# Kernel optimization log

Measured on AMD Instinct MI355X. Metric: run time of the kernel, lower is better.

The kernel has to match this reference:

```python
import jax, jax.numpy as jnp
import numpy as np

B, C, H, W = 8, 256, 128, 128
NUM_HEADS = 8
EPS = 1e-6


def setup_inputs() -> dict:
    key = jax.random.key(0)
    ks = jax.random.split(key, 7)
    s = 1.0 / np.sqrt(C)
    return {
        "x": jax.random.normal(ks[0], (B, C, H, W), dtype=jnp.float32),
        "Wq": jax.random.normal(ks[1], (C, C), dtype=jnp.float32) * s,
        "bq": jax.random.normal(ks[2], (C,), dtype=jnp.float32) * 0.01,
        "Wk": jax.random.normal(ks[3], (C, C), dtype=jnp.float32) * s,
        "bk": jax.random.normal(ks[4], (C,), dtype=jnp.float32) * 0.01,
        "Wv": jax.random.normal(ks[5], (C, C), dtype=jnp.float32) * s,
        "bv": jax.random.normal(ks[6], (C,), dtype=jnp.float32) * 0.01,
    }


def reference(x, Wq, bq, Wk, bk, Wv, bv):
    b, c_full, h_sp, w_sp = x.shape
    p = NUM_HEADS
    c = c_full // p  # per-head channels
    n = h_sp * w_sp  # spatial tokens

    def proj(Wm, bm):
        # 1x1 conv == channel-mixing linear: out[b,o,h,w] = sum_c W[o,c]*x[b,c,h,w] + b[o]
        return jnp.einsum('bchw,oc->bohw', x, Wm) + bm[None, :, None, None]

    q = jax.nn.softplus(proj(Wq, bq)).reshape(b, p, c, n).transpose(0, 1, 3, 2)  # [b,p,n,c]
    k = jax.nn.softplus(proj(Wk, bk)).reshape(b, p, c, n)                        # [b,p,c,n]
    v = proj(Wv, bv).reshape(b, p, c, n)                                         # [b,p,c,n]

    # KV accumulation: [b,p,c_k,c_v] (small)
    kv = jnp.einsum('bpmn,bpcn->bpmc', k, v)
    # normalization: 1 / (q . (sum_n k + eps))
    norm = 1.0 / jnp.einsum('bpnc,bpc->bpn', q, jnp.sum(k, axis=-1) + EPS)
    out = jnp.einsum('bpnm,bpmc,bpn->bpcn', q, kv, norm)  # [b,p,c,n]
    return out.reshape(b, c_full, h_sp, w_sp)
```

## Files before the change

kernel.cpp:

```cpp
#include <hip/hip_runtime.h>
#include <hip/hip_bf16.h>
#include <math.h>

#define BATCH 8
#define CFULL 256
#define HEADS 8
#define CH 32
#define NTOK 16384
#define TN 64
#define TTN 32
#define KSLD 40
#define EPS 1e-6f

#define SWZ(tok) ((((tok) & 7) << 3) ^ ((((tok) >> 3) & 3) << 6))

typedef __bf16 bf16x8 __attribute__((ext_vector_type(8)));
typedef float f32x4 __attribute__((ext_vector_type(4)));
typedef float f32x16 __attribute__((ext_vector_type(16)));
typedef float fvec4 __attribute__((ext_vector_type(4)));
typedef unsigned short ushort8v __attribute__((ext_vector_type(8)));
typedef int int4v __attribute__((ext_vector_type(4)));

__device__ __forceinline__ unsigned short bf16bits(float f) {
    return __builtin_bit_cast(unsigned short, (__bf16)f);
}
__device__ __forceinline__ float softplus_f(float x) {
    return fmaxf(x, 0.0f) + __logf(1.0f + __expf(-fabsf(x)));
}

__device__ __forceinline__ void quad_transpose(fvec4& a, int lane) {
    const bool o1 = lane & 1, o2 = lane & 2;
    float s1 = o1 ? a.x : a.y; float g1 = __shfl_xor(s1, 1);
    float s2 = o1 ? a.z : a.w; float g2 = __shfl_xor(s2, 1);
    a.x = o1 ? g1 : a.x;  a.y = o1 ? a.y : g1;
    a.z = o1 ? g2 : a.z;  a.w = o1 ? a.w : g2;
    float s3 = o2 ? a.x : a.z; float g3 = __shfl_xor(s3, 2);
    float s4 = o2 ? a.y : a.w; float g4 = __shfl_xor(s4, 2);
    a.x = o2 ? g3 : a.x;  a.z = o2 ? a.z : g3;
    a.y = o2 ? g4 : a.y;  a.w = o2 ? a.w : g4;
}

template <int NW>
__device__ __forceinline__ void stage_x(const float* __restrict__ xb, int n0,
                                        unsigned short* xs, int wv, int lane) {
    const int q4 = lane & 3;
    const int t0 = (lane >> 2) << 2;
    constexpr int G = 64 / NW;
    #pragma unroll
    for (int g = 0; g < G; ++g) {
        const int c0 = wv * (G * 4) + g * 4;
        fvec4 a = __builtin_nontemporal_load(
            (const fvec4*)(xb + (size_t)(c0 + q4) * NTOK + n0 + t0));
        quad_transpose(a, lane);
        ushort4 pk;
        pk.x = bf16bits(a.x); pk.y = bf16bits(a.y);
        pk.z = bf16bits(a.z); pk.w = bf16bits(a.w);
        *(ushort4*)&xs[lane * CFULL + (c0 ^ SWZ(lane))] = pk;
    }
}

template <int NW>
__device__ __forceinline__ void stage_tile(const unsigned short* __restrict__ xTb,
                                           int n0, unsigned short* xs, int wv, int lane) {
    constexpr int R = 64 / NW;
    const unsigned short* src = xTb + (size_t)(n0 + wv * R) * CFULL + lane * 8;
    unsigned short* dst = &xs[wv * R * CFULL];
    #pragma unroll
    for (int i = 0; i < R / 2; ++i) {
        __builtin_amdgcn_global_load_lds(
            (const __attribute__((address_space(1))) unsigned int*)(src + i * 512),
            (__attribute__((address_space(3))) unsigned int*)(dst + i * 512),
            16, 0, 0);
    }
}

__device__ __forceinline__ void stage32(const unsigned short* __restrict__ xTb,
                                        int n0, unsigned short* buf, int wv, int lane) {
    const unsigned short* src = xTb + (size_t)(n0 + wv * 4) * CFULL + lane * 8;
    unsigned short* dst = buf + wv * 4 * CFULL;
    #pragma unroll
    for (int i = 0; i < 2; ++i) {
        __builtin_amdgcn_global_load_lds(
            (const __attribute__((address_space(1))) unsigned int*)(src + i * 512),
            (__attribute__((address_space(3))) unsigned int*)(dst + i * 512),
            16, 0, 0);
    }
}

__global__ void prep_w(const float* __restrict__ Wq, const float* __restrict__ Wk,
                       const float* __restrict__ Wv, unsigned short* __restrict__ dst)
{
    const int i = blockIdx.x * 256 + threadIdx.x;
    const float* src = (i < 65536) ? Wq : ((i < 131072) ? Wk : Wv);
    dst[i] = bf16bits(src[i & 65535]);
}

__global__ __launch_bounds__(512)
void xpose(const float* __restrict__ x, unsigned short* __restrict__ xT)
{
    __shared__ __align__(16) unsigned short xs[TN * CFULL];
    const int tid = threadIdx.x;
    const int lane = tid & 63;
    const int wv = tid >> 6;
    const int b = blockIdx.x >> 8;
    const int n0 = (blockIdx.x & 255) * TN;

    stage_x<8>(x + (size_t)b * CFULL * NTOK, n0, xs, wv, lane);
    __syncthreads();
    int4v* dst = (int4v*)(xT + ((size_t)b * NTOK + n0) * CFULL);
    const int4v* src = (const int4v*)xs;
    #pragma unroll
    for (int i = 0; i < 4; ++i)
        dst[i * 512 + tid] = src[i * 512 + tid];
}

__global__ __launch_bounds__(512)
void k1_kv(const unsigned short* __restrict__ xT,
           const unsigned short* __restrict__ Wk,
           const unsigned short* __restrict__ Wv,
           const float* __restrict__ bk, const float* __restrict__ bv,
           float* __restrict__ kvpart, float* __restrict__ kspart,
           int bpb, int ntiles)
{
    __shared__ __align__(16) unsigned short xs0[TTN * CFULL];
    __shared__ __align__(16) unsigned short xs1[TTN * CFULL];
    __shared__ __align__(16) unsigned short ks[CFULL * KSLD];
    __shared__ __align__(16) unsigned short vs[CFULL * KSLD];

    const int tid = threadIdx.x;
    const int lane = tid & 63;
    const int wv = tid >> 6;
    const int l15 = lane & 15;
    const int lhi = lane >> 4;
    const int bid = blockIdx.x;
    const int b = bid / bpb;
    const int blk = bid % bpb;
    const int tokbase = blk * (ntiles * TTN);
    const unsigned short* xTb = xT + (size_t)b * NTOK * CFULL;

    float bkr[2], bvr[2];
    #pragma unroll
    for (int of = 0; of < 2; ++of) {
        bkr[of] = bk[wv * 32 + of * 16 + l15];
        bvr[of] = bv[wv * 32 + of * 16 + l15];
    }

    f32x16 kvacc = {};
    float ksum[2] = {0.f, 0.f};

    stage32(xTb, tokbase, xs0, wv, lane);
    __syncthreads();

    for (int t = 0; t < ntiles; ++t) {
        unsigned short* cur = (t & 1) ? xs1 : xs0;
        unsigned short* nxt = (t & 1) ? xs0 : xs1;
        if (t + 1 < ntiles)
            stage32(xTb, tokbase + (t + 1) * TTN, nxt, wv, lane);

        {
            f32x4 acc[2][2] = {};
            #pragma unroll
            for (int kk = 0; kk < 8; ++kk) {
                const int ch0 = kk * 32 + lhi * 8;
                bf16x8 af[2], bfr[2];
                #pragma unroll
                for (int tf = 0; tf < 2; ++tf) {
                    const int tok = tf * 16 + l15;
                    af[tf] = *(const bf16x8*)&cur[tok * CFULL + (ch0 ^ SWZ(tok))];
                }
                #pragma unroll
                for (int of = 0; of < 2; ++of) {
                    const int och = wv * 32 + of * 16 + l15;
                    bfr[of] = *(const bf16x8*)&Wk[och * CFULL + ch0];
                }
                #pragma unroll
                for (int tf = 0; tf < 2; ++tf)
                    #pragma unroll
                    for (int of = 0; of < 2; ++of)
                        acc[tf][of] = __builtin_amdgcn_mfma_f32_16x16x32_bf16(af[tf], bfr[of], acc[tf][of], 0, 0, 0);
            }
            #pragma unroll
            for (int tf = 0; tf < 2; ++tf) {
                #pragma unroll
                for (int of = 0; of < 2; ++of) {
                    const int och = wv * 32 + of * 16 + l15;
                    const float bias = bkr[of];
                    float v0 = softplus_f(acc[tf][of][0] + bias);
                    float v1 = softplus_f(acc[tf][of][1] + bias);
                    float v2 = softplus_f(acc[tf][of][2] + bias);
                    float v3 = softplus_f(acc[tf][of][3] + bias);
                    ksum[of] += v0 + v1 + v2 + v3;
                    ushort4 pk;
                    pk.x = bf16bits(v0); pk.y = bf16bits(v1);
                    pk.z = bf16bits(v2); pk.w = bf16bits(v3);
                    *(ushort4*)&ks[och * KSLD + tf * 16 + lhi * 4] = pk;
                }
            }
        }

        {
            f32x4 acc[2][2] = {};
            #pragma unroll
            for (int kk = 0; kk < 8; ++kk) {
                const int ch0 = kk * 32 + lhi * 8;
                bf16x8 af[2], bfr[2];
                #pragma unroll
                for (int tf = 0; tf < 2; ++tf) {
                    const int tok = tf * 16 + l15;
                    af[tf] = *(const bf16x8*)&cur[tok * CFULL + (ch0 ^ SWZ(tok))];
                }
                #pragma unroll
                for (int of = 0; of < 2; ++of) {
                    const int och = wv * 32 + of * 16 + l15;
                    bfr[of] = *(const bf16x8*)&Wv[och * CFULL + ch0];
                }
                #pragma unroll
                for (int tf = 0; tf < 2; ++tf)
                    #pragma unroll
                    for (int of = 0; of < 2; ++of)
                        acc[tf][of] = __builtin_amdgcn_mfma_f32_16x16x32_bf16(af[tf], bfr[of], acc[tf][of], 0, 0, 0);
            }
            #pragma unroll
            for (int tf = 0; tf < 2; ++tf) {
                #pragma unroll
                for (int of = 0; of < 2; ++of) {
                    const int och = wv * 32 + of * 16 + l15;
                    const float bias = bvr[of];
                    ushort4 pk;
                    pk.x = bf16bits(acc[tf][of][0] + bias);
                    pk.y = bf16bits(acc[tf][of][1] + bias);
                    pk.z = bf16bits(acc[tf][of][2] + bias);
                    pk.w = bf16bits(acc[tf][of][3] + bias);
                    *(ushort4*)&vs[och * KSLD + tf * 16 + lhi * 4] = pk;
                }
            }
        }

        {
            const int l31 = lane & 31;
            const int hi = lane >> 5;
            const int row = wv * 32 + l31;
            #pragma unroll
            for (int ts = 0; ts < 2; ++ts) {
                const int sw = ts * 16 + hi * 8;
                bf16x8 ak = *(const bf16x8*)&ks[row * KSLD + sw];
                bf16x8 av = *(const bf16x8*)&vs[row * KSLD + sw];
                kvacc = __builtin_amdgcn_mfma_f32_32x32x16_bf16(ak, av, kvacc, 0, 0, 0);
            }
        }

        __syncthreads();
    }

    #pragma unroll
    for (int of = 0; of < 2; ++of) {
        float v = ksum[of];
        v += __shfl_xor(v, 16);
        v += __shfl_xor(v, 32);
        if (lhi == 0) kspart[bid * CFULL + wv * 32 + of * 16 + l15] = v;
    }
    {
        float* kvp = kvpart + ((size_t)bid << 13);
        const int l31 = lane & 31;
        const int hi = lane >> 5;
        #pragma unroll
        for (int q = 0; q < 4; ++q) {
            const int m0 = 8 * q + 4 * hi;
            f32x4 s;
            s[0] = kvacc[4 * q + 0]; s[1] = kvacc[4 * q + 1];
            s[2] = kvacc[4 * q + 2]; s[3] = kvacc[4 * q + 3];
            *(f32x4*)&kvp[wv * 1024 + l31 * 32 + m0] = s;
        }
    }
}

__global__ __launch_bounds__(256)
void k1r(const float* __restrict__ kvpart, const float* __restrict__ kspart,
         unsigned short* __restrict__ kvT, float* __restrict__ kse, int bpb)
{
    const int o = blockIdx.x * 256 + threadIdx.x;
    const int b = o >> 13;
    const int r = o & 8191;
    float s = 0.f;
    for (int j = 0; j < bpb; ++j)
        s += kvpart[((size_t)(b * bpb + j) << 13) + r];
    kvT[o] = bf16bits(s);
    if (blockIdx.x < BATCH) {
        const int bb = blockIdx.x;
        float t = 0.f;
        for (int j = 0; j < bpb; ++j)
            t += kspart[(bb * bpb + j) * CFULL + threadIdx.x];
        kse[bb * CFULL + threadIdx.x] = t + EPS;
    }
}

__global__ __launch_bounds__(512)
void k2_out(const unsigned short* __restrict__ xT,
            const unsigned short* __restrict__ Wq,
            const float* __restrict__ bq,
            const unsigned short* __restrict__ kvT, const float* __restrict__ ksef,
            float* __restrict__ outp)
{
    __shared__ __align__(16) unsigned short xs[TN * CFULL];
    __shared__ float normls[HEADS][TN];

    const int tid = threadIdx.x;
    const int lane = tid & 63;
    const int wv = tid >> 6;
    const int l15 = lane & 15;
    const int lhi = lane >> 4;
    const int b = blockIdx.x >> 8;
    const int blk = blockIdx.x & 255;
    const int n0 = blk * TN;
    float* ob = outp + (size_t)b * CFULL * NTOK;

    stage_tile<8>(xT + (size_t)b * NTOK * CFULL, n0, xs, wv, lane);

    bf16x8 awr[2][8];
    #pragma unroll
    for (int of = 0; of < 2; ++of) {
        const unsigned short* wrow = Wq + (size_t)(wv * 32 + of * 16 + l15) * CFULL + lhi * 8;
        #pragma unroll
        for (int kk = 0; kk < 8; ++kk)
            awr[of][kk] = *(const bf16x8*)&wrow[kk * 32];
    }
    bf16x8 bh[2];
    {
        const int base = (b * HEADS + wv) << 10;
        #pragma unroll
        for (int hf = 0; hf < 2; ++hf)
            bh[hf] = *(const bf16x8*)&kvT[base + (hf * 16 + l15) * 32 + lhi * 8];
    }
    float bq0[2][4], ksq[2][4];
    #pragma unroll
    for (int of = 0; of < 2; ++of) {
        const int och0 = wv * 32 + of * 16 + lhi * 4;
        #pragma unroll
        for (int r = 0; r < 4; ++r) {
            bq0[of][r] = bq[och0 + r];
            ksq[of][r] = ksef[b * CFULL + och0 + r];
        }
    }

    __syncthreads();

    f32x4 acc[2][4] = {};
    #pragma unroll
    for (int kk = 0; kk < 8; ++kk) {
        const int ch0 = kk * 32 + lhi * 8;
        bf16x8 bx[4];
        #pragma unroll
        for (int nf = 0; nf < 4; ++nf) {
            const int tok = nf * 16 + l15;
            bx[nf] = *(const bf16x8*)&xs[tok * CFULL + (ch0 ^ SWZ(tok))];
        }
        #pragma unroll
        for (int of = 0; of < 2; ++of)
            #pragma unroll
            for (int nf = 0; nf < 4; ++nf)
                acc[of][nf] = __builtin_amdgcn_mfma_f32_16x16x32_bf16(awr[of][kk], bx[nf], acc[of][nf], 0, 0, 0);
    }
    __syncthreads();

    float dpart[4] = {0.f, 0.f, 0.f, 0.f};
    #pragma unroll
    for (int of = 0; of < 2; ++of) {
        #pragma unroll
        for (int nf = 0; nf < 4; ++nf) {
            float q0 = softplus_f(acc[of][nf][0] + bq0[of][0]);
            float q1 = softplus_f(acc[of][nf][1] + bq0[of][1]);
            float q2 = softplus_f(acc[of][nf][2] + bq0[of][2]);
            float q3 = softplus_f(acc[of][nf][3] + bq0[of][3]);
            dpart[nf] += q0 * ksq[of][0] + q1 * ksq[of][1] +
                         q2 * ksq[of][2] + q3 * ksq[of][3];
            ushort4 pk;
            pk.x = bf16bits(q0); pk.y = bf16bits(q1);
            pk.z = bf16bits(q2); pk.w = bf16bits(q3);
            const int tok = nf * 16 + l15;
            const int och0 = wv * 32 + of * 16 + lhi * 4;
            *(ushort4*)&xs[tok * CFULL + (och0 ^ SWZ(tok))] = pk;
        }
    }
    #pragma unroll
    for (int nf = 0; nf < 4; ++nf) {
        float d = dpart[nf];
        d += __shfl_xor(d, 16);
        d += __shfl_xor(d, 32);
        if (lhi == 0) normls[wv][nf * 16 + l15] = 1.0f / d;
    }

    #pragma unroll
    for (int nf = 0; nf < 4; ++nf) {
        const int tok = nf * 16 + l15;
        bf16x8 af = *(const bf16x8*)&xs[tok * CFULL + ((wv * 32 + lhi * 8) ^ SWZ(tok))];
        f32x4 oA = {}, oB = {};
        oA = __builtin_amdgcn_mfma_f32_16x16x32_bf16(af, bh[0], oA, 0, 0, 0);
        oB = __builtin_amdgcn_mfma_f32_16x16x32_bf16(af, bh[1], oB, 0, 0, 0);
        const int tb = nf * 16 + lhi * 4;
        const f32x4 nrm = *(const f32x4*)&normls[wv][tb];
        f32x4 sA, sB;
        sA[0] = oA[0] * nrm[0]; sA[1] = oA[1] * nrm[1];
        sA[2] = oA[2] * nrm[2]; sA[3] = oA[3] * nrm[3];
        sB[0] = oB[0] * nrm[0]; sB[1] = oB[1] * nrm[1];
        sB[2] = oB[2] * nrm[2]; sB[3] = oB[3] * nrm[3];
        *(f32x4*)&ob[(size_t)(wv * 32 + l15) * NTOK + n0 + tb] = sA;
        *(f32x4*)&ob[(size_t)(wv * 32 + 16 + l15) * NTOK + n0 + tb] = sB;
    }
}

extern "C" void kernel_launch(void* const* d_in, const int* in_sizes, int n_in,
                              void* d_out, int out_size, void* d_ws, size_t ws_size,
                              hipStream_t stream)
{
    const float* x  = (const float*)d_in[0];
    const float* Wq = (const float*)d_in[1];
    const float* bq = (const float*)d_in[2];
    const float* Wk = (const float*)d_in[3];
    const float* bk = (const float*)d_in[4];
    const float* Wv = (const float*)d_in[5];
    const float* bv = (const float*)d_in[6];
    float* out = (float*)d_out;

    unsigned char* ws = (unsigned char*)d_ws;
    unsigned short* wbf = (unsigned short*)ws;
    unsigned short* kvT = (unsigned short*)(ws + 393216);
    float* kse = (float*)(ws + 524288);

    const size_t xT_sz = (size_t)BATCH * NTOK * CFULL * 2;

    int bpb = 64;
    size_t ksp_off = 532480;
    size_t kvp_off = ksp_off + (size_t)BATCH * bpb * CFULL * 4;
    size_t kvp_sz  = (size_t)BATCH * bpb * 8192 * 4;
    if (ws_size < kvp_off + kvp_sz + xT_sz) {
        bpb = 16;
        kvp_off = ksp_off + (size_t)BATCH * bpb * CFULL * 4;
        kvp_sz  = (size_t)BATCH * bpb * 8192 * 4;
    }
    float* kspart = (float*)(ws + ksp_off);
    float* kvpart = (float*)(ws + kvp_off);
    unsigned short* xT = (unsigned short*)(ws + kvp_off + kvp_sz);
    const int ntiles = NTOK / TTN / bpb;

    hipLaunchKernelGGL(prep_w, dim3(768), dim3(256), 0, stream, Wq, Wk, Wv, wbf);
    hipLaunchKernelGGL(xpose, dim3(BATCH * 256), dim3(512), 0, stream, x, xT);
    hipLaunchKernelGGL(k1_kv, dim3(BATCH * bpb), dim3(512), 0, stream,
                       xT, wbf + 65536, wbf + 2 * 65536, bk, bv,
                       kvpart, kspart, bpb, ntiles);
    hipLaunchKernelGGL(k1r, dim3(256), dim3(256), 0, stream,
                       kvpart, kspart, kvT, kse, bpb);
    hipLaunchKernelGGL(k2_out, dim3(BATCH * 256), dim3(512), 0, stream,
                       xT, wbf, bq, kvT, kse, out);
}
```

Measured before the change: 214.1 us.

## Make output kernel persistent with double-buffered 32-token tiles

```diff
diff --git a/kernel.cpp b/kernel.cpp
--- a/kernel.cpp
+++ b/kernel.cpp
@@ -299,31 +299,27 @@
             const unsigned short* __restrict__ Wq,
             const float* __restrict__ bq,
             const unsigned short* __restrict__ kvT, const float* __restrict__ ksef,
-            float* __restrict__ outp)
-{
-    __shared__ __align__(16) unsigned short xs[TN * CFULL];
-    __shared__ float normls[HEADS][TN];
+            float* __restrict__ outp, int bpb, int ntiles)
+{
+    __shared__ __align__(16) unsigned short xs0[TTN * CFULL];
+    __shared__ __align__(16) unsigned short xs1[TTN * CFULL];
+    __shared__ __align__(16) unsigned short qs[TTN * CFULL];
+    __shared__ float normls[HEADS][TTN];
 
     const int tid = threadIdx.x;
     const int lane = tid & 63;
     const int wv = tid >> 6;
     const int l15 = lane & 15;
     const int lhi = lane >> 4;
-    const int b = blockIdx.x >> 8;
-    const int blk = blockIdx.x & 255;
-    const int n0 = blk * TN;
+    const int bid = blockIdx.x;
+    const int b = bid / bpb;
+    const int blk = bid % bpb;
+    const int tokbase = blk * (ntiles * TTN);
+    const unsigned short* xTb = xT + (size_t)b * NTOK * CFULL;
     float* ob = outp + (size_t)b * CFULL * NTOK;
 
-    stage_tile<8>(xT + (size_t)b * NTOK * CFULL, n0, xs, wv, lane);
-
-    bf16x8 awr[2][8];
-    #pragma unroll
-    for (int of = 0; of < 2; ++of) {
-        const unsigned short* wrow = Wq + (size_t)(wv * 32 + of * 16 + l15) * CFULL + lhi * 8;
-        #pragma unroll
-        for (int kk = 0; kk < 8; ++kk)
-            awr[of][kk] = *(const bf16x8*)&wrow[kk * 32];
-    }
+    stage32(xTb, tokbase, xs0, wv, lane);
+
     bf16x8 bh[2];
     {
         const int base = (b * HEADS + wv) << 10;
@@ -344,67 +340,79 @@
 
     __syncthreads();
 
-    f32x4 acc[2][4] = {};
-    #pragma unroll
-    for (int kk = 0; kk < 8; ++kk) {
-        const int ch0 = kk * 32 + lhi * 8;
-        bf16x8 bx[4];
-        #pragma unroll
-        for (int nf = 0; nf < 4; ++nf) {
+    for (int t = 0; t < ntiles; ++t) {
+        unsigned short* cur = (t & 1) ? xs1 : xs0;
+        unsigned short* nxt = (t & 1) ? xs0 : xs1;
+        if (t + 1 < ntiles)
+            stage32(xTb, tokbase + (t + 1) * TTN, nxt, wv, lane);
+        const int n0 = tokbase + t * TTN;
+
+        f32x4 acc[2][2] = {};
+        #pragma unroll
+        for (int kk = 0; kk < 8; ++kk) {
+            const int ch0 = kk * 32 + lhi * 8;
+            bf16x8 aw[2], bx[2];
+            #pragma unroll
+            for (int of = 0; of < 2; ++of)
+                aw[of] = *(const bf16x8*)&Wq[(wv * 32 + of * 16 + l15) * CFULL + ch0];
+            #pragma unroll
+            for (int nf = 0; nf < 2; ++nf) {
+                const int tok = nf * 16 + l15;
+                bx[nf] = *(const bf16x8*)&cur[tok * CFULL + (ch0 ^ SWZ(tok))];
+            }
+            #pragma unroll
+            for (int of = 0; of < 2; ++of)
+                #pragma unroll
+                for (int nf = 0; nf < 2; ++nf)
+                    acc[of][nf] = __builtin_amdgcn_mfma_f32_16x16x32_bf16(aw[of], bx[nf], acc[of][nf], 0, 0, 0);
+        }
+
+        float dpart[2] = {0.f, 0.f};
+        #pragma unroll
+        for (int of = 0; of < 2; ++of) {
+            #pragma unroll
+            for (int nf = 0; nf < 2; ++nf) {
+                float q0 = softplus_f(acc[of][nf][0] + bq0[of][0]);
+                float q1 = softplus_f(acc[of][nf][1] + bq0[of][1]);
+                float q2 = softplus_f(acc[of][nf][2] + bq0[of][2]);
+                float q3 = softplus_f(acc[of][nf][3] + bq0[of][3]);
+                dpart[nf] += q0 * ksq[of][0] + q1 * ksq[of][1] +
+                             q2 * ksq[of][2] + q3 * ksq[of][3];
+                ushort4 pk;
+                pk.x = bf16bits(q0); pk.y = bf16bits(q1);
+                pk.z = bf16bits(q2); pk.w = bf16bits(q3);
+                const int tok = nf * 16 + l15;
+                const int och0 = wv * 32 + of * 16 + lhi * 4;
+                *(ushort4*)&qs[tok * CFULL + (och0 ^ SWZ(tok))] = pk;
+            }
+        }
+        #pragma unroll
+        for (int nf = 0; nf < 2; ++nf) {
+            float d = dpart[nf];
+            d += __shfl_xor(d, 16);
+            d += __shfl_xor(d, 32);
+            if (lhi == 0) normls[wv][nf * 16 + l15] = 1.0f / d;
+        }
+
+        #pragma unroll
+        for (int nf = 0; nf < 2; ++nf) {
             const int tok = nf * 16 + l15;
-            bx[nf] = *(const bf16x8*)&xs[tok * CFULL + (ch0 ^ SWZ(tok))];
-        }
-        #pragma unroll
-        for (int of = 0; of < 2; ++of)
-            #pragma unroll
-            for (int nf = 0; nf < 4; ++nf)
-                acc[of][nf] = __builtin_amdgcn_mfma_f32_16x16x32_bf16(awr[of][kk], bx[nf], acc[of][nf], 0, 0, 0);
-    }
-    __syncthreads();
-
-    float dpart[4] = {0.f, 0.f, 0.f, 0.f};
-    #pragma unroll
-    for (int of = 0; of < 2; ++of) {
-        #pragma unroll
-        for (int nf = 0; nf < 4; ++nf) {
-            float q0 = softplus_f(acc[of][nf][0] + bq0[of][0]);
-            float q1 = softplus_f(acc[of][nf][1] + bq0[of][1]);
-            float q2 = softplus_f(acc[of][nf][2] + bq0[of][2]);
-            float q3 = softplus_f(acc[of][nf][3] + bq0[of][3]);
-            dpart[nf] += q0 * ksq[of][0] + q1 * ksq[of][1] +
-                         q2 * ksq[of][2] + q3 * ksq[of][3];
-            ushort4 pk;
-            pk.x = bf16bits(q0); pk.y = bf16bits(q1);
-            pk.z = bf16bits(q2); pk.w = bf16bits(q3);
-            const int tok = nf * 16 + l15;
-            const int och0 = wv * 32 + of * 16 + lhi * 4;
-            *(ushort4*)&xs[tok * CFULL + (och0 ^ SWZ(tok))] = pk;
-        }
-    }
-    #pragma unroll
-    for (int nf = 0; nf < 4; ++nf) {
-        float d = dpart[nf];
-        d += __shfl_xor(d, 16);
-        d += __shfl_xor(d, 32);
-        if (lhi == 0) normls[wv][nf * 16 + l15] = 1.0f / d;
-    }
-
-    #pragma unroll
-    for (int nf = 0; nf < 4; ++nf) {
-        const int tok = nf * 16 + l15;
-        bf16x8 af = *(const bf16x8*)&xs[tok * CFULL + ((wv * 32 + lhi * 8) ^ SWZ(tok))];
-        f32x4 oA = {}, oB = {};
-        oA = __builtin_amdgcn_mfma_f32_16x16x32_bf16(af, bh[0], oA, 0, 0, 0);
-        oB = __builtin_amdgcn_mfma_f32_16x16x32_bf16(af, bh[1], oB, 0, 0, 0);
-        const int tb = nf * 16 + lhi * 4;
-        const f32x4 nrm = *(const f32x4*)&normls[wv][tb];
-        f32x4 sA, sB;
-        sA[0] = oA[0] * nrm[0]; sA[1] = oA[1] * nrm[1];
-        sA[2] = oA[2] * nrm[2]; sA[3] = oA[3] * nrm[3];
-        sB[0] = oB[0] * nrm[0]; sB[1] = oB[1] * nrm[1];
-        sB[2] = oB[2] * nrm[2]; sB[3] = oB[3] * nrm[3];
-        *(f32x4*)&ob[(size_t)(wv * 32 + l15) * NTOK + n0 + tb] = sA;
-        *(f32x4*)&ob[(size_t)(wv * 32 + 16 + l15) * NTOK + n0 + tb] = sB;
+            bf16x8 af = *(const bf16x8*)&qs[tok * CFULL + ((wv * 32 + lhi * 8) ^ SWZ(tok))];
+            f32x4 oA = {}, oB = {};
+            oA = __builtin_amdgcn_mfma_f32_16x16x32_bf16(af, bh[0], oA, 0, 0, 0);
+            oB = __builtin_amdgcn_mfma_f32_16x16x32_bf16(af, bh[1], oB, 0, 0, 0);
+            const int tb = nf * 16 + lhi * 4;
+            const f32x4 nrm = *(const f32x4*)&normls[wv][tb];
+            f32x4 sA, sB;
+            sA[0] = oA[0] * nrm[0]; sA[1] = oA[1] * nrm[1];
+            sA[2] = oA[2] * nrm[2]; sA[3] = oA[3] * nrm[3];
+            sB[0] = oB[0] * nrm[0]; sB[1] = oB[1] * nrm[1];
+            sB[2] = oB[2] * nrm[2]; sB[3] = oB[3] * nrm[3];
+            *(f32x4*)&ob[(size_t)(wv * 32 + l15) * NTOK + n0 + tb] = sA;
+            *(f32x4*)&ob[(size_t)(wv * 32 + 16 + l15) * NTOK + n0 + tb] = sB;
+        }
+
+        __syncthreads();
     }
 }
 
@@ -442,6 +450,9 @@
     unsigned short* xT = (unsigned short*)(ws + kvp_off + kvp_sz);
     const int ntiles = NTOK / TTN / bpb;
 
+    const int bpb2 = 128;
+    const int ntiles2 = NTOK / TTN / bpb2;
+
     hipLaunchKernelGGL(prep_w, dim3(768), dim3(256), 0, stream, Wq, Wk, Wv, wbf);
     hipLaunchKernelGGL(xpose, dim3(BATCH * 256), dim3(512), 0, stream, x, xT);
     hipLaunchKernelGGL(k1_kv, dim3(BATCH * bpb), dim3(512), 0, stream,
@@ -449,6 +460,6 @@
                        kvpart, kspart, bpb, ntiles);
     hipLaunchKernelGGL(k1r, dim3(256), dim3(256), 0, stream,
                        kvpart, kspart, kvT, kse, bpb);
-    hipLaunchKernelGGL(k2_out, dim3(BATCH * 256), dim3(512), 0, stream,
-                       xT, wbf, bq, kvT, kse, out);
-}
+    hipLaunchKernelGGL(k2_out, dim3(BATCH * bpb2), dim3(512), 0, stream,
+                       xT, wbf, bq, kvT, kse, out, bpb2, ntiles2);
+}
```

New measurement: 199.2 us. 6.9% less time.
